# Kernel optimization log

Measured on AMD Instinct MI355X. Metric: run time of the kernel, lower is better.

Reference implementation:

```python
import jax, jax.numpy as jnp
import numpy as np

N, E, IN, K, F, D = 50000, 800000, 256, 4, 64, 2


def setup_inputs() -> dict:
    key = jax.random.key(0)
    ks = jax.random.split(key, 10)
    # CSR rowptr: 0 .. E, nondecreasing, endpoints pinned
    inner = jnp.sort(jax.random.randint(ks[0], (N - 1,), 0, E + 1))
    rowptr = jnp.concatenate([jnp.zeros(1, jnp.int64), inner.astype(jnp.int64), jnp.full(1, E, jnp.int64)])
    colind = jax.random.randint(ks[1], (E,), 0, N).astype(jnp.int64)
    # CSC mirrors (used only by the fused kernel's backward; inert in forward math)
    inner_c = jnp.sort(jax.random.randint(ks[2], (N - 1,), 0, E + 1))
    colptr = jnp.concatenate([jnp.zeros(1, jnp.int64), inner_c.astype(jnp.int64), jnp.full(1, E, jnp.int64)])
    rowind = jax.random.randint(ks[3], (E,), 0, N).astype(jnp.int64)
    permute = jnp.arange(E, dtype=jnp.int64)
    feat = jax.random.normal(ks[4], (N, IN), dtype=jnp.float32)
    pseudo = jax.random.uniform(ks[5], (E, D), dtype=jnp.float32)
    # params: fc weight [K*F, IN] (xavier-normal style scale), mu ~ N(0, 0.1), inv_sigma = 1, bias = 0
    gain = float(np.sqrt(2.0))
    std = gain * float(np.sqrt(2.0 / (IN + K * F)))
    W_fc = jax.random.normal(ks[6], (K * F, IN), dtype=jnp.float32) * std
    mu = jax.random.normal(ks[7], (K, D), dtype=jnp.float32) * 0.1
    inv_sigma = jnp.ones((K, D), dtype=jnp.float32)
    bias = jnp.zeros((F,), dtype=jnp.float32)
    return {"rowptr": rowptr, "colind": colind, "colptr": colptr, "rowind": rowind,
            "permute": permute, "feat": feat, "pseudo": pseudo,
            "W_fc": W_fc, "mu": mu, "inv_sigma": inv_sigma, "bias": bias}


def reference(rowptr, colind, colptr, rowind, permute, feat, pseudo, W_fc, mu, inv_sigma, bias):
    n = feat.shape[0]
    e = colind.shape[0]
    k, d = mu.shape
    f = W_fc.shape[0] // k
    # dense projection: [N, K, F]
    node_feat = (feat @ W_fc.T).reshape(n, k, f)
    # per-edge Gaussian mixture weights: [E, K]
    diff = pseudo[:, None, :] - mu[None, :, :]              # [E, K, D]
    gaussian = jnp.exp(jnp.sum(-0.5 * diff * diff * (inv_sigma[None, :, :] ** 2), axis=-1))
    # multi-head SpMM: gather source feats, weight per kernel, sum kernels (sum commutes
    # with the segment reduction, so fold the head-sum into the edge message): [E, F]
    msg = jnp.einsum('ek,ekf->ef', gaussian, node_feat[colind])
    # destination node of each CSR edge
    dst = jnp.searchsorted(rowptr, jnp.arange(e), side='right') - 1
    rst = jax.ops.segment_sum(msg, dst, num_segments=n)      # [N, F]
    return rst + bias
```

## Files before the change

kernel.cpp:

```cpp
#include <hip/hip_runtime.h>


typedef __attribute__((ext_vector_type(8))) short bf16x8;
typedef __attribute__((ext_vector_type(4))) float f32x4;

__device__ inline unsigned short f32_to_bf16(float f) {
    union { float f; unsigned int u; } c; c.f = f;
    unsigned int u = c.u;
    u += 0x7fffu + ((u >> 16) & 1u);
    return (unsigned short)(u >> 16);
}
__device__ inline float bf16_to_f32(unsigned short h) {
    union { unsigned int u; float f; } c; c.u = ((unsigned int)h) << 16;
    return c.f;
}
__device__ inline ushort4 cvt4(float4 v) {
    ushort4 h;
    h.x = f32_to_bf16(v.x); h.y = f32_to_bf16(v.y);
    h.z = f32_to_bf16(v.z); h.w = f32_to_bf16(v.w);
    return h;
}

__global__ __launch_bounds__(256) void convert_inputs(
    const float* __restrict__ W, const float* __restrict__ feat,
    unsigned short* __restrict__ Wp, unsigned short* __restrict__ Af,
    int nFeat4)
{
    const int gid = blockIdx.x * 256 + threadIdx.x;
    if (gid < 16384) {
        const int jp = gid >> 6, k4 = gid & 63;
        const int wrow = ((jp & 3) << 6) | (jp >> 2);
        reinterpret_cast<ushort4*>(Wp)[jp * 64 + k4] =
            cvt4(reinterpret_cast<const float4*>(W)[wrow * 64 + k4]);
    }
    for (int i = gid; i < nFeat4; i += gridDim.x * 256)
        reinterpret_cast<ushort4*>(Af)[i] =
            cvt4(reinterpret_cast<const float4*>(feat)[i]);
}

__global__ __launch_bounds__(256) void gemm_inplace(
    unsigned short* AC,
    const unsigned short* __restrict__ Wp,
    int M)
{
    __shared__ unsigned short As[64 * 32];
    __shared__ unsigned short Bs[256 * 32];
    const int t    = threadIdx.x;
    const int lane = t & 63;
    const int wave = t >> 6;
    const int bm   = blockIdx.x * 64;
    const int l16  = lane & 15;
    const int quad = lane >> 4;
    const int wn   = wave * 64;

    const int kc   = (lane & 3) * 8;
    const int arow = min(bm + wave * 16 + (lane >> 2), M - 1);
    const size_t asrc = (size_t)arow * 256 + kc;
    size_t bsrc[4];
#pragma unroll
    for (int j = 0; j < 4; ++j)
        bsrc[j] = (size_t)(wave * 64 + j * 16 + (lane >> 2)) * 256 + kc;

    f32x4 acc[4][4];
#pragma unroll
    for (int mi = 0; mi < 4; ++mi)
#pragma unroll
        for (int ni = 0; ni < 4; ++ni)
            acc[mi][ni] = (f32x4){0.f, 0.f, 0.f, 0.f};

    typedef __attribute__((address_space(3))) void lds_t;
    typedef const __attribute__((address_space(1))) void gm_t;

    for (int k0 = 0; k0 < 256; k0 += 32) {
        __builtin_amdgcn_global_load_lds((gm_t*)(AC + asrc + k0),
            (lds_t*)(As + wave * 512), 16, 0, 0);
#pragma unroll
        for (int j = 0; j < 4; ++j)
            __builtin_amdgcn_global_load_lds((gm_t*)(Wp + bsrc[j] + k0),
                (lds_t*)(Bs + (wave * 4 + j) * 512), 16, 0, 0);
        __syncthreads();

        bf16x8 af[4], bfr[4];
#pragma unroll
        for (int mi = 0; mi < 4; ++mi)
            af[mi] = *reinterpret_cast<const bf16x8*>(
                &As[(mi * 16 + l16) * 32 + quad * 8]);
#pragma unroll
        for (int ni = 0; ni < 4; ++ni)
            bfr[ni] = *reinterpret_cast<const bf16x8*>(
                &Bs[(wn + ni * 16 + l16) * 32 + quad * 8]);
#pragma unroll
        for (int mi = 0; mi < 4; ++mi)
#pragma unroll
            for (int ni = 0; ni < 4; ++ni)
                acc[mi][ni] = __builtin_amdgcn_mfma_f32_16x16x32_bf16(
                    af[mi], bfr[ni], acc[mi][ni], 0, 0, 0);
        __syncthreads();
    }

#pragma unroll
    for (int mi = 0; mi < 4; ++mi) {
#pragma unroll
        for (int r = 0; r < 4; ++r) {
            const int row = bm + mi * 16 + quad * 4 + r;
            if (row < M) {
#pragma unroll
                for (int ni = 0; ni < 4; ++ni) {
                    const int col = wn + ni * 16 + l16;
                    AC[(size_t)row * 256 + col] = f32_to_bf16(acc[mi][ni][r]);
                }
            }
        }
    }
}

__global__ __launch_bounds__(128) void edge_aggregate(
    const int* __restrict__ rowptr,
    const int* __restrict__ colind,
    const float* __restrict__ pseudo,
    const unsigned short* __restrict__ nf,
    const float* __restrict__ mu,
    const float* __restrict__ inv_sigma,
    const float* __restrict__ bias,
    float* __restrict__ out,
    int N)
{
    __shared__ float gbuf[2][64];
    __shared__ int   cbuf[2][16];
    const int wave = threadIdx.x >> 6;
    const int lane = threadIdx.x & 63;
    const int node = blockIdx.x * 2 + wave;
    if (node >= N) return;

    const int kk = lane >> 4;
    const int ii = lane & 15;
    const float mx = mu[2 * kk], my = mu[2 * kk + 1];
    const float sa = inv_sigma[2 * kk], sb = inv_sigma[2 * kk + 1];
    const float sx = sa * sa, sy = sb * sb;

    const int e0 = rowptr[node];
    const int e1 = rowptr[node + 1];
    float* gw = gbuf[wave];
    int*   cw = cbuf[wave];

    float acc = 0.f;
    for (int ec = e0; ec < e1; ec += 16) {
        const int cnt = min(16, e1 - ec);
        {
            const bool v = ii < cnt;
            const int e = v ? (ec + ii) : e0;
            const float2 p = *reinterpret_cast<const float2*>(pseudo + 2 * (size_t)e);
            const float dx = p.x - mx, dy = p.y - my;
            const float g = v ? __expf(-0.5f * (dx * dx * sx + dy * dy * sy)) : 0.f;
            gw[ii * 4 + kk] = g;
            if (kk == 0) cw[ii] = v ? colind[e] : 0;
        }
        __builtin_amdgcn_wave_barrier();
        __threadfence_block();
        const int cnt4 = (cnt + 3) & ~3;
        for (int i2 = 0; i2 < cnt4; i2 += 4) {
            const int c0 = cw[i2 + 0], c1 = cw[i2 + 1];
            const int c2 = cw[i2 + 2], c3 = cw[i2 + 3];
            const ushort4 h0 = *reinterpret_cast<const ushort4*>(nf + ((size_t)c0 << 8) + (lane << 2));
            const ushort4 h1 = *reinterpret_cast<const ushort4*>(nf + ((size_t)c1 << 8) + (lane << 2));
            const ushort4 h2 = *reinterpret_cast<const ushort4*>(nf + ((size_t)c2 << 8) + (lane << 2));
            const ushort4 h3 = *reinterpret_cast<const ushort4*>(nf + ((size_t)c3 << 8) + (lane << 2));
            const float4 g0 = *reinterpret_cast<const float4*>(&gw[(i2 + 0) * 4]);
            const float4 g1 = *reinterpret_cast<const float4*>(&gw[(i2 + 1) * 4]);
            const float4 g2 = *reinterpret_cast<const float4*>(&gw[(i2 + 2) * 4]);
            const float4 g3 = *reinterpret_cast<const float4*>(&gw[(i2 + 3) * 4]);
            acc += g0.x * bf16_to_f32(h0.x) + g0.y * bf16_to_f32(h0.y)
                 + g0.z * bf16_to_f32(h0.z) + g0.w * bf16_to_f32(h0.w);
            acc += g1.x * bf16_to_f32(h1.x) + g1.y * bf16_to_f32(h1.y)
                 + g1.z * bf16_to_f32(h1.z) + g1.w * bf16_to_f32(h1.w);
            acc += g2.x * bf16_to_f32(h2.x) + g2.y * bf16_to_f32(h2.y)
                 + g2.z * bf16_to_f32(h2.z) + g2.w * bf16_to_f32(h2.w);
            acc += g3.x * bf16_to_f32(h3.x) + g3.y * bf16_to_f32(h3.y)
                 + g3.z * bf16_to_f32(h3.z) + g3.w * bf16_to_f32(h3.w);
        }
        __builtin_amdgcn_wave_barrier();
        __threadfence_block();
    }
    out[((size_t)node << 6) + lane] = acc + bias[lane];
}

extern "C" void kernel_launch(void* const* d_in, const int* in_sizes, int n_in,
                              void* d_out, int out_size, void* d_ws, size_t ws_size,
                              hipStream_t stream)
{
    const int*   rowptr    = (const int*)d_in[0];
    const int*   colind    = (const int*)d_in[1];
    const float* feat      = (const float*)d_in[5];
    const float* pseudo    = (const float*)d_in[6];
    const float* W_fc      = (const float*)d_in[7];
    const float* mu        = (const float*)d_in[8];
    const float* inv_sigma = (const float*)d_in[9];
    const float* bias      = (const float*)d_in[10];
    float* out = (float*)d_out;

    const int N = in_sizes[0] - 1;
    unsigned short* AC = (unsigned short*)d_ws;
    unsigned short* Wp = (unsigned short*)d_out;

    hipLaunchKernelGGL(convert_inputs, dim3(1024), dim3(256), 0, stream,
                       W_fc, feat, Wp, AC, N * 64);

    hipLaunchKernelGGL(gemm_inplace, dim3((N + 63) / 64), dim3(256), 0, stream,
                       AC, Wp, N);

    hipLaunchKernelGGL(edge_aggregate, dim3((N + 1) / 2), dim3(128), 0, stream,
                       rowptr, colind, pseudo, AC, mu, inv_sigma, bias, out, N);
}
```

Measured before the change: 199.1 us.

## Fuse feat fp32-to-bf16 conversion into GEMM and restage A tile in LDS

```diff
diff --git a/kernel.cpp b/kernel.cpp
--- a/kernel.cpp
+++ b/kernel.cpp
@@ -21,29 +21,25 @@
     return h;
 }
 
-__global__ __launch_bounds__(256) void convert_inputs(
-    const float* __restrict__ W, const float* __restrict__ feat,
-    unsigned short* __restrict__ Wp, unsigned short* __restrict__ Af,
-    int nFeat4)
+__global__ __launch_bounds__(256) void convert_W(
+    const float* __restrict__ W, unsigned short* __restrict__ Wp)
 {
     const int gid = blockIdx.x * 256 + threadIdx.x;
-    if (gid < 16384) {
-        const int jp = gid >> 6, k4 = gid & 63;
-        const int wrow = ((jp & 3) << 6) | (jp >> 2);
-        reinterpret_cast<ushort4*>(Wp)[jp * 64 + k4] =
-            cvt4(reinterpret_cast<const float4*>(W)[wrow * 64 + k4]);
-    }
-    for (int i = gid; i < nFeat4; i += gridDim.x * 256)
-        reinterpret_cast<ushort4*>(Af)[i] =
-            cvt4(reinterpret_cast<const float4*>(feat)[i]);
-}
-
-__global__ __launch_bounds__(256) void gemm_inplace(
-    unsigned short* AC,
+    const int jp = gid >> 6, k4 = gid & 63;
+    const int wrow = ((jp & 3) << 6) | (jp >> 2);
+    reinterpret_cast<ushort4*>(Wp)[jp * 64 + k4] =
+        cvt4(reinterpret_cast<const float4*>(W)[wrow * 64 + k4]);
+}
+
+#define ASTRIDE 264
+
+__global__ __launch_bounds__(256) void gemm_fused(
+    const float* __restrict__ feat,
     const unsigned short* __restrict__ Wp,
+    unsigned short* __restrict__ nf,
     int M)
 {
-    __shared__ unsigned short As[64 * 32];
+    __shared__ unsigned short As[64 * ASTRIDE];
     __shared__ unsigned short Bs[256 * 32];
     const int t    = threadIdx.x;
     const int lane = t & 63;
@@ -53,13 +49,30 @@
     const int quad = lane >> 4;
     const int wn   = wave * 64;
 
-    const int kc   = (lane & 3) * 8;
-    const int arow = min(bm + wave * 16 + (lane >> 2), M - 1);
-    const size_t asrc = (size_t)arow * 256 + kc;
     size_t bsrc[4];
 #pragma unroll
     for (int j = 0; j < 4; ++j)
-        bsrc[j] = (size_t)(wave * 64 + j * 16 + (lane >> 2)) * 256 + kc;
+        bsrc[j] = (size_t)(wave * 64 + j * 16 + (lane >> 2)) * 256 + (lane & 3) * 8;
+
+    typedef __attribute__((address_space(3))) void lds_t;
+    typedef const __attribute__((address_space(1))) void gm_t;
+
+#pragma unroll
+    for (int j = 0; j < 4; ++j)
+        __builtin_amdgcn_global_load_lds((gm_t*)(Wp + bsrc[j]),
+            (lds_t*)(Bs + (wave * 4 + j) * 512), 16, 0, 0);
+
+#pragma unroll
+    for (int it = 0; it < 8; ++it) {
+        const int flat = it * 2048 + t * 8;
+        const int row  = flat >> 8;
+        const int koff = flat & 255;
+        const float* src = feat + (size_t)min(bm + row, M - 1) * 256 + koff;
+        const float4 a0 = *reinterpret_cast<const float4*>(src);
+        const float4 a1 = *reinterpret_cast<const float4*>(src + 4);
+        *reinterpret_cast<ushort4*>(&As[row * ASTRIDE + koff])     = cvt4(a0);
+        *reinterpret_cast<ushort4*>(&As[row * ASTRIDE + koff + 4]) = cvt4(a1);
+    }
 
     f32x4 acc[4][4];
 #pragma unroll
@@ -68,34 +81,33 @@
         for (int ni = 0; ni < 4; ++ni)
             acc[mi][ni] = (f32x4){0.f, 0.f, 0.f, 0.f};
 
-    typedef __attribute__((address_space(3))) void lds_t;
-    typedef const __attribute__((address_space(1))) void gm_t;
-
-    for (int k0 = 0; k0 < 256; k0 += 32) {
-        __builtin_amdgcn_global_load_lds((gm_t*)(AC + asrc + k0),
-            (lds_t*)(As + wave * 512), 16, 0, 0);
-#pragma unroll
-        for (int j = 0; j < 4; ++j)
-            __builtin_amdgcn_global_load_lds((gm_t*)(Wp + bsrc[j] + k0),
-                (lds_t*)(Bs + (wave * 4 + j) * 512), 16, 0, 0);
+    for (int ki = 0; ki < 8; ++ki) {
         __syncthreads();
 
         bf16x8 af[4], bfr[4];
 #pragma unroll
         for (int mi = 0; mi < 4; ++mi)
             af[mi] = *reinterpret_cast<const bf16x8*>(
-                &As[(mi * 16 + l16) * 32 + quad * 8]);
+                &As[(mi * 16 + l16) * ASTRIDE + ki * 32 + quad * 8]);
 #pragma unroll
         for (int ni = 0; ni < 4; ++ni)
             bfr[ni] = *reinterpret_cast<const bf16x8*>(
                 &Bs[(wn + ni * 16 + l16) * 32 + quad * 8]);
+
+        __syncthreads();
+        if (ki < 7) {
+            const int k0 = (ki + 1) * 32;
+#pragma unroll
+            for (int j = 0; j < 4; ++j)
+                __builtin_amdgcn_global_load_lds((gm_t*)(Wp + bsrc[j] + k0),
+                    (lds_t*)(Bs + (wave * 4 + j) * 512), 16, 0, 0);
+        }
 #pragma unroll
         for (int mi = 0; mi < 4; ++mi)
 #pragma unroll
             for (int ni = 0; ni < 4; ++ni)
                 acc[mi][ni] = __builtin_amdgcn_mfma_f32_16x16x32_bf16(
                     af[mi], bfr[ni], acc[mi][ni], 0, 0, 0);
-        __syncthreads();
     }
 
 #pragma unroll
@@ -107,7 +119,7 @@
 #pragma unroll
                 for (int ni = 0; ni < 4; ++ni) {
                     const int col = wn + ni * 16 + l16;
-                    AC[(size_t)row * 256 + col] = f32_to_bf16(acc[mi][ni][r]);
+                    nf[(size_t)row * 256 + col] = f32_to_bf16(acc[mi][ni][r]);
                 }
             }
         }
@@ -199,15 +211,14 @@
     float* out = (float*)d_out;
 
     const int N = in_sizes[0] - 1;
-    unsigned short* AC = (unsigned short*)d_ws;
+    unsigned short* nf = (unsigned short*)d_ws;
     unsigned short* Wp = (unsigned short*)d_out;
 
-    hipLaunchKernelGGL(convert_inputs, dim3(1024), dim3(256), 0, stream,
-                       W_fc, feat, Wp, AC, N * 64);
-
-    hipLaunchKernelGGL(gemm_inplace, dim3((N + 63) / 64), dim3(256), 0, stream,
-                       AC, Wp, N);
+    hipLaunchKernelGGL(convert_W, dim3(64), dim3(256), 0, stream, W_fc, Wp);
+
+    hipLaunchKernelGGL(gemm_fused, dim3((N + 63) / 64), dim3(256), 0, stream,
+                       feat, Wp, nf, N);
 
     hipLaunchKernelGGL(edge_aggregate, dim3((N + 1) / 2), dim3(128), 0, stream,
-                       rowptr, colind, pseudo, AC, mu, inv_sigma, bias, out, N);
-}
+                       rowptr, colind, pseudo, nf, mu, inv_sigma, bias, out, N);
+}
```

New measurement: 192.0 us. -3.5%, faster.
